# Kernel tuning notes

Measured on AMD Instinct MI355X. Metric: run time of the kernel, lower is better.

## Reference

```python
import jax, jax.numpy as jnp
import numpy as np

B, T, D, H, DH, FF = 512, 64, 512, 8, 64, 2048
SCALE = DH ** -0.5  # head_dim ** -0.5


def _ln(x, g, b):
    m = x.mean(-1, keepdims=True)
    v = x.var(-1, keepdims=True)
    return (x - m) / jnp.sqrt(v + 1e-5) * g + b


def _l2n(x):
    return x / jnp.maximum(jnp.linalg.norm(x, axis=-1, keepdims=True), 1e-12)


def setup_inputs() -> dict:
    key = jax.random.key(0)
    ks = jax.random.split(key, 16)

    def w(k, shape):
        fan_in = shape[0]
        return jax.random.normal(k, shape, jnp.float32) / np.sqrt(fan_in).astype(np.float32)

    return {
        'item_seq': jax.random.normal(ks[0], (B, T, D), jnp.float32),
        'user_static_emb': jax.random.normal(ks[1], (B, D), jnp.float32),
        'last_item_emb': jax.random.normal(ks[2], (B, D), jnp.float32),
        'init_state': jnp.zeros((B, H, DH, DH), jnp.float32),
        'Wq': w(ks[3], (D, D)), 'Wk': w(ks[4], (D, D)), 'Wv': w(ks[5], (D, D)),
        'Wa': w(ks[6], (D, H)), 'ba': jnp.zeros((H,), jnp.float32),
        'We': w(ks[7], (D, H)), 'be': jnp.zeros((H,), jnp.float32),
        'mcW1': w(ks[8], (2 * D, D)), 'mcb1': jnp.zeros((D,), jnp.float32),
        'mcg': jnp.ones((D,), jnp.float32), 'mcbt': jnp.zeros((D,), jnp.float32),
        'mcW2': w(ks[9], (D, 2 * D + 2 * H)), 'mcb2': jnp.zeros((2 * D + 2 * H,), jnp.float32),
        'Wo': w(ks[10], (D, D)), 'bo': jnp.zeros((D,), jnp.float32),
        'W1': w(ks[11], (D, FF)), 'b1': jnp.zeros((FF,), jnp.float32),
        'W2': w(ks[12], (FF, D)), 'b2': jnp.zeros((D,), jnp.float32),
        'n1g': jnp.ones((D,), jnp.float32), 'n1b': jnp.zeros((D,), jnp.float32),
        'n2g': jnp.ones((D,), jnp.float32), 'n2b': jnp.zeros((D,), jnp.float32),
    }


def reference(item_seq, user_static_emb, last_item_emb, init_state,
              Wq, Wk, Wv, Wa, ba, We, be,
              mcW1, mcb1, mcg, mcbt, mcW2, mcb2,
              Wo, bo, W1, b1, W2, b2, n1g, n1b, n2g, n2b):
    def read(q_emb, state):
        # q: (B,H,Dh) L2-normalized; read = S @ q per head
        q = _l2n((q_emb @ Wq).reshape(-1, H, DH))
        return jnp.einsum('bhij,bhj->bhi', state, q).reshape(-1, D)

    us_norm = _ln(user_static_emb, n1g, n1b)  # constant across steps

    def step(state, item):
        i_norm = _ln(item, n1g, n1b)
        mem_ctx = read(i_norm, state)
        meta_in = jnp.concatenate([us_norm, mem_ctx], axis=-1)
        h = jax.nn.relu(_ln(meta_in @ mcW1 + mcb1, mcg, mcbt))
        mo = h @ mcW2 + mcb2
        gamma, beta = mo[:, :D], mo[:, D:2 * D]
        alpha_bias, eta_bias = mo[:, 2 * D:2 * D + H], mo[:, 2 * D + H:]
        mod = i_norm * (1.0 + jnp.tanh(gamma)) + beta
        k = _l2n((mod @ Wk).reshape(-1, H, DH))
        v = (mod @ Wv).reshape(-1, H, DH)
        alpha = jax.nn.sigmoid(mod @ Wa + ba + alpha_bias)[:, :, None, None]
        eta = (jax.nn.sigmoid(mod @ We + be + eta_bias) * SCALE)[:, :, None, None]
        pred = jnp.einsum('bhij,bhj->bhi', state, k)
        upd = jnp.einsum('bhi,bhj->bhij', v - pred, k)  # rank-1 outer-product write
        return (1.0 - alpha) * state + eta * upd, None

    state, _ = jax.lax.scan(step, init_state, jnp.swapaxes(item_seq, 0, 1))

    # predict (read) path
    q_norm = _ln(last_item_emb, n1g, n1b)
    attn = read(q_norm, state) @ Wo + bo
    x = user_static_emb + attn
    x2 = _ln(x, n2g, n2b)
    ffn = jax.nn.relu(x2 @ W1 + b1) @ W2 + b2
    return x + ffn
```

## Files before the change

kernel.cpp:

```cpp
#include <hip/hip_runtime.h>
#include <cmath>

constexpr int cB = 512, cT = 64, cD = 512, cH = 8, cDH = 64, cFF = 2048;
constexpr float cSCALE = 0.125f;

typedef short bfrag __attribute__((ext_vector_type(8)));
typedef float f32x4 __attribute__((ext_vector_type(4)));

__device__ __forceinline__ short f2bf(float x) {
  union { float f; unsigned u; } v{x};
  unsigned r = v.u + 0x7fff + ((v.u >> 16) & 1);
  return (short)(r >> 16);
}
__device__ __forceinline__ float bf2f(short s) {
  union { unsigned u; float f; } v;
  v.u = ((unsigned)(unsigned short)s) << 16;
  return v.f;
}
__device__ __forceinline__ float sigm(float z) { return 1.f / (1.f + __expf(-z)); }

enum GemmMode { MQ = 0, MWO, MFF1, MFF2 };

struct GemmArgs {
  const float *A, *A2, *sm, *sr, *g, *b;
  const short *WT, *WT2;
  const float *bias, *extra;
  float *O;
  short *Os;
};

template<int MODE>
__device__ __forceinline__ float loadA(const GemmArgs& p, int r, int k) {
  if constexpr (MODE == MQ) {
    int t = r >> 9, bb = r & 511;
    float v = (t < cT) ? p.A[((size_t)bb * cT + t) * cD + k]
                       : p.A2[(size_t)bb * cD + k];
    return (v - p.sm[r]) * p.sr[r] * p.g[k] + p.b[k];
  } else if constexpr (MODE == MFF1) {
    return (p.A[(size_t)r * cD + k] - p.sm[r]) * p.sr[r] * p.g[k] + p.b[k];
  } else if constexpr (MODE == MFF2) {
    return p.A[(size_t)r * cFF + k];
  } else {
    return p.A[(size_t)r * cD + k];
  }
}

template<int MODE>
__device__ __forceinline__ void epi(const GemmArgs& p, int r, int cn, float acc) {
  if constexpr (MODE == MQ) {
    p.Os[(size_t)r * cD + cn] = f2bf(acc);
  } else if constexpr (MODE == MWO) {
    p.O[(size_t)r * cD + cn] = p.extra[(size_t)r * cD + cn] + acc + p.bias[cn];
  } else if constexpr (MODE == MFF1) {
    p.O[(size_t)r * cFF + cn] = fmaxf(acc + p.bias[cn], 0.f);
  } else {
    p.O[(size_t)r * cD + cn] = p.extra[(size_t)r * cD + cn] + acc + p.bias[cn];
  }
}

template<int MODE, int LDW>
__global__ __launch_bounds__(256) void mgemm(GemmArgs p, int K) {
  __shared__ short As[64][32];
  __shared__ short Bs[64][32];
  const int tid = threadIdx.x;
  const int lane = tid & 63, wid = tid >> 6;
  const int wm = wid & 1, wn = wid >> 1;
  const int l15 = lane & 15, qd = lane >> 4;
  const int row0 = blockIdx.x * 64;
  const int n0 = blockIdx.y * 64;

  f32x4 acc[2][2] = {};
  const int sm = tid >> 2;
  const int sk = (tid & 3) * 8;

  for (int k0 = 0; k0 < K; k0 += 32) {
    {
      short tmp[8];
#pragma unroll
      for (int j = 0; j < 8; ++j)
        tmp[j] = f2bf(loadA<MODE>(p, row0 + sm, k0 + sk + j));
      *((bfrag*)&As[sm][0] + (sk >> 3)) = *(bfrag*)tmp;
    }
    *((bfrag*)&Bs[sm][0] + (sk >> 3)) =
        *(const bfrag*)(p.WT + (size_t)(n0 + sm) * LDW + k0 + sk);
    __syncthreads();
    bfrag a0 = *((bfrag*)&As[wm * 32 + l15][0] + qd);
    bfrag a1 = *((bfrag*)&As[wm * 32 + 16 + l15][0] + qd);
    bfrag b0 = *((bfrag*)&Bs[wn * 32 + l15][0] + qd);
    bfrag b1 = *((bfrag*)&Bs[wn * 32 + 16 + l15][0] + qd);
    acc[0][0] = __builtin_amdgcn_mfma_f32_16x16x32_bf16(a0, b0, acc[0][0], 0, 0, 0);
    acc[0][1] = __builtin_amdgcn_mfma_f32_16x16x32_bf16(a0, b1, acc[0][1], 0, 0, 0);
    acc[1][0] = __builtin_amdgcn_mfma_f32_16x16x32_bf16(a1, b0, acc[1][0], 0, 0, 0);
    acc[1][1] = __builtin_amdgcn_mfma_f32_16x16x32_bf16(a1, b1, acc[1][1], 0, 0, 0);
    __syncthreads();
  }

#pragma unroll
  for (int fm = 0; fm < 2; ++fm)
#pragma unroll
    for (int fn = 0; fn < 2; ++fn)
#pragma unroll
      for (int rg = 0; rg < 4; ++rg)
        epi<MODE>(p, row0 + wm * 32 + fm * 16 + qd * 4 + rg,
                  n0 + wn * 32 + fn * 16 + l15, acc[fm][fn][rg]);
}

template<int MODE, int LDW>
__global__ __launch_bounds__(256) void pgemm(GemmArgs p, int K) {
  __shared__ short Ah[64][32], Al[64][32];
  __shared__ short Bh[64][32], Bl[64][32];
  const int tid = threadIdx.x;
  const int lane = tid & 63, wid = tid >> 6;
  const int wm = wid & 1, wn = wid >> 1;
  const int l15 = lane & 15, qd = lane >> 4;
  const int row0 = blockIdx.x * 64;
  const int n0 = blockIdx.y * 64;

  f32x4 acc[2][2] = {};
  const int sm = tid >> 2;
  const int sk = (tid & 3) * 8;

  for (int k0 = 0; k0 < K; k0 += 32) {
    {
      short th[8], tl[8];
#pragma unroll
      for (int j = 0; j < 8; ++j) {
        float a = loadA<MODE>(p, row0 + sm, k0 + sk + j);
        short h = f2bf(a);
        th[j] = h;
        tl[j] = f2bf(a - bf2f(h));
      }
      *((bfrag*)&Ah[sm][0] + (sk >> 3)) = *(bfrag*)th;
      *((bfrag*)&Al[sm][0] + (sk >> 3)) = *(bfrag*)tl;
    }
    *((bfrag*)&Bh[sm][0] + (sk >> 3)) =
        *(const bfrag*)(p.WT + (size_t)(n0 + sm) * LDW + k0 + sk);
    *((bfrag*)&Bl[sm][0] + (sk >> 3)) =
        *(const bfrag*)(p.WT2 + (size_t)(n0 + sm) * LDW + k0 + sk);
    __syncthreads();
#pragma unroll
    for (int fm = 0; fm < 2; ++fm) {
      bfrag ah = *((bfrag*)&Ah[wm * 32 + fm * 16 + l15][0] + qd);
      bfrag al = *((bfrag*)&Al[wm * 32 + fm * 16 + l15][0] + qd);
#pragma unroll
      for (int fn = 0; fn < 2; ++fn) {
        bfrag bh = *((bfrag*)&Bh[wn * 32 + fn * 16 + l15][0] + qd);
        bfrag bl = *((bfrag*)&Bl[wn * 32 + fn * 16 + l15][0] + qd);
        acc[fm][fn] = __builtin_amdgcn_mfma_f32_16x16x32_bf16(al, bh, acc[fm][fn], 0, 0, 0);
        acc[fm][fn] = __builtin_amdgcn_mfma_f32_16x16x32_bf16(ah, bl, acc[fm][fn], 0, 0, 0);
        acc[fm][fn] = __builtin_amdgcn_mfma_f32_16x16x32_bf16(ah, bh, acc[fm][fn], 0, 0, 0);
      }
    }
    __syncthreads();
  }

#pragma unroll
  for (int fm = 0; fm < 2; ++fm)
#pragma unroll
    for (int fn = 0; fn < 2; ++fn)
#pragma unroll
      for (int rg = 0; rg < 4; ++rg)
        epi<MODE>(p, row0 + wm * 32 + fm * 16 + qd * 4 + rg,
                  n0 + wn * 32 + fn * 16 + l15, acc[fm][fn][rg]);
}

__global__ __launch_bounds__(256) void tconv(const float* __restrict__ W,
                                             short* __restrict__ WT, int K, int N) {
  __shared__ float tile[32][33];
  int k0 = blockIdx.x * 32, n0 = blockIdx.y * 32;
  int tx = threadIdx.x & 31, ty = threadIdx.x >> 5;
#pragma unroll
  for (int j = 0; j < 32; j += 8) {
    int k = k0 + ty + j, n = n0 + tx;
    tile[ty + j][tx] = (k < K && n < N) ? W[(size_t)k * N + n] : 0.f;
  }
  __syncthreads();
#pragma unroll
  for (int j = 0; j < 32; j += 8) {
    int n = n0 + ty + j, k = k0 + tx;
    if (n < N && k < K) WT[(size_t)n * K + k] = f2bf(tile[tx][ty + j]);
  }
}

__global__ __launch_bounds__(256) void tconv2(const float* __restrict__ W,
                                              short* __restrict__ WTh,
                                              short* __restrict__ WTl, int K, int N) {
  __shared__ float tile[32][33];
  int k0 = blockIdx.x * 32, n0 = blockIdx.y * 32;
  int tx = threadIdx.x & 31, ty = threadIdx.x >> 5;
#pragma unroll
  for (int j = 0; j < 32; j += 8) {
    int k = k0 + ty + j, n = n0 + tx;
    tile[ty + j][tx] = (k < K && n < N) ? W[(size_t)k * N + n] : 0.f;
  }
  __syncthreads();
#pragma unroll
  for (int j = 0; j < 32; j += 8) {
    int n = n0 + ty + j, k = k0 + tx;
    if (n < N && k < K) {
      float v = tile[tx][ty + j];
      short h = f2bf(v);
      WTh[(size_t)n * K + k] = h;
      WTl[(size_t)n * K + k] = f2bf(v - bf2f(h));
    }
  }
}

__global__ __launch_bounds__(256) void ln_stats_k(
    const float* __restrict__ item_seq, const float* __restrict__ last_item,
    const float* __restrict__ user, const float* __restrict__ n1g,
    const float* __restrict__ n1b, float* __restrict__ lnm,
    float* __restrict__ lnr, float* __restrict__ us_norm) {
  const int lane = threadIdx.x & 63;
  const int w = blockIdx.x * 4 + (threadIdx.x >> 6);
  const float* src;
  int cls, bi = 0;
  if (w < cT * cB) {
    int t = w >> 9, bb = w & 511;
    src = item_seq + ((size_t)bb * cT + t) * cD;
    cls = 0;
  } else if (w < cT * cB + cB) {
    bi = w - cT * cB;
    src = last_item + (size_t)bi * cD;
    cls = 1;
  } else {
    bi = w - cT * cB - cB;
    src = user + (size_t)bi * cD;
    cls = 2;
  }
  float x[8], s = 0.f, ss = 0.f;
#pragma unroll
  for (int i = 0; i < 8; ++i) {
    float v = src[lane + i * 64];
    x[i] = v; s += v; ss += v * v;
  }
#pragma unroll
  for (int o = 32; o >= 1; o >>= 1) { s += __shfl_xor(s, o); ss += __shfl_xor(ss, o); }
  float m = s * (1.f / cD);
  float rstd = rsqrtf(ss * (1.f / cD) - m * m + 1e-5f);
  if (cls == 0) {
    if (lane == 0) { lnm[w] = m; lnr[w] = rstd; }
  } else if (cls == 1) {
    if (lane == 0) { lnm[cT * cB + bi] = m; lnr[cT * cB + bi] = rstd; }
  } else {
#pragma unroll
    for (int i = 0; i < 8; ++i) {
      int d = lane + i * 64;
      us_norm[(size_t)bi * cD + d] = (x[i] - m) * rstd * n1g[d] + n1b[d];
    }
  }
}

__global__ __launch_bounds__(256) void row_stats_k(const float* __restrict__ X,
                                                   float* __restrict__ M,
                                                   float* __restrict__ R) {
  const int lane = threadIdx.x & 63;
  const int w = blockIdx.x * 4 + (threadIdx.x >> 6);
  float s = 0.f, ss = 0.f;
#pragma unroll
  for (int i = 0; i < 8; ++i) {
    float v = X[(size_t)w * cD + lane + i * 64];
    s += v; ss += v * v;
  }
#pragma unroll
  for (int o = 32; o >= 1; o >>= 1) { s += __shfl_xor(s, o); ss += __shfl_xor(ss, o); }
  if (lane == 0) {
    float m = s * (1.f / cD);
    M[w] = m;
    R[w] = rsqrtf(ss * (1.f / cD) - m * m + 1e-5f);
  }
}

struct Scan2Params {
  const float *item_seq, *init_state, *us_norm, *lnm, *lnr, *n1g, *n1b;
  const float *mcb1, *mcg, *mcbt, *mcb2, *ba, *be;
  const short *wt_m1, *wt_m2, *wt_k, *wt_v, *wt_ae, *q_all;
  float *mem_ctx;
};

__device__ __forceinline__ bfrag mk_afrag(const float* xr, int kc, int qd) {
  const float* s = xr + kc * 32 + qd * 8;
  float4 a = *(const float4*)s;
  float4 b = *(const float4*)(s + 4);
  short t[8] = {f2bf(a.x), f2bf(a.y), f2bf(a.z), f2bf(a.w),
                f2bf(b.x), f2bf(b.y), f2bf(b.z), f2bf(b.w)};
  return *(bfrag*)t;
}

__global__ __launch_bounds__(1024, 4) void scan2_k(Scan2Params p) {
  const int tid = threadIdx.x;
  const int lane = tid & 63, w = tid >> 6;
  const int bb = w >> 3, h = w & 7;
  const int l15 = lane & 15, qd = lane >> 4;
  const int b0 = blockIdx.x * 2;

  __shared__ float xcat[2][1024];
  __shared__ float rbuf[2][512];
  __shared__ float x2b[2][512];
  __shared__ float mo[2][1040];
  __shared__ float modv[2][512];
  __shared__ float kvb[2][1024];
  __shared__ float khat[16][64];
  __shared__ float qh[16][64];
  __shared__ float aeta[2][8][2];
  __shared__ float st[2][2], st2[2][2];
  __shared__ float cb1[512], cg[512], cbt[512], cb2[1040];
  __shared__ float cn1g[512], cn1b[512], cba[8], cbe[8];

  if (tid < 512) {
    cb1[tid] = p.mcb1[tid]; cg[tid] = p.mcg[tid]; cbt[tid] = p.mcbt[tid];
    cn1g[tid] = p.n1g[tid]; cn1b[tid] = p.n1b[tid];
  }
  cb2[tid] = p.mcb2[tid];
  if (tid < 16) cb2[1024 + tid] = p.mcb2[1024 + tid];
  if (tid < 8) { cba[tid] = p.ba[tid]; cbe[tid] = p.be[tid]; }
  {
    int row = tid >> 9, c = tid & 511;
    xcat[row][c] = p.us_norm[(size_t)(b0 + row) * cD + c];
  }

  float S[64];
  {
    const float* sp = p.init_state + ((((size_t)(b0 + bb)) * cH + h) * cDH + lane) * cDH;
#pragma unroll
    for (int j = 0; j < 64; j += 4) {
      float4 t4 = *(const float4*)(sp + j);
      S[j] = t4.x; S[j + 1] = t4.y; S[j + 2] = t4.z; S[j + 3] = t4.w;
    }
  }
  float memv;
  {
    float qv = bf2f(p.q_all[(size_t)(b0 + bb) * cD + h * cDH + lane]);
    float qs = qv * qv;
#pragma unroll
    for (int o = 32; o >= 1; o >>= 1) qs += __shfl_xor(qs, o);
    qh[w][lane] = qv / fmaxf(sqrtf(qs), 1e-12f);
    memv = 0.f;
#pragma unroll
    for (int j = 0; j < 64; j += 4) {
      float4 q4 = *(const float4*)&qh[w][j];
      memv += S[j] * q4.x + S[j + 1] * q4.y + S[j + 2] * q4.z + S[j + 3] * q4.w;
    }
    xcat[bb][512 + h * cDH + lane] = memv;
  }
  __syncthreads();

  for (int t = 0; t < cT; ++t) {
    {
      f32x4 a0 = {}, a1 = {};
      const int n0 = w * 16, n1 = (w + 16) * 16;
#pragma unroll 4
      for (int kc = 0; kc < 32; ++kc) {
        bfrag A = {};
        if (l15 < 2) A = mk_afrag(&xcat[l15][0], kc, qd);
        bfrag B0 = *(const bfrag*)(p.wt_m1 + (size_t)(n0 + l15) * 1024 + kc * 32 + qd * 8);
        bfrag B1 = *(const bfrag*)(p.wt_m1 + (size_t)(n1 + l15) * 1024 + kc * 32 + qd * 8);
        a0 = __builtin_amdgcn_mfma_f32_16x16x32_bf16(A, B0, a0, 0, 0, 0);
        a1 = __builtin_amdgcn_mfma_f32_16x16x32_bf16(A, B1, a1, 0, 0, 0);
      }
      if (lane < 16) {
        rbuf[0][n0 + lane] = a0[0] + cb1[n0 + lane];
        rbuf[1][n0 + lane] = a0[1] + cb1[n0 + lane];
        rbuf[0][n1 + lane] = a1[0] + cb1[n1 + lane];
        rbuf[1][n1 + lane] = a1[1] + cb1[n1 + lane];
      }
    }
    __syncthreads();
    if (w < 2) {
      float s = 0.f, ss = 0.f;
#pragma unroll
      for (int i = 0; i < 8; ++i) { float v = rbuf[w][lane + i * 64]; s += v; ss += v * v; }
#pragma unroll
      for (int o = 32; o >= 1; o >>= 1) { s += __shfl_xor(s, o); ss += __shfl_xor(ss, o); }
      if (lane == 0) {
        float m = s * (1.f / cD);
        st[w][0] = m;
        st[w][1] = rsqrtf(ss * (1.f / cD) - m * m + 1e-5f);
      }
    } else if (w == 2 && lane < 2) {
      st2[lane][0] = p.lnm[t * cB + b0 + lane];
      st2[lane][1] = p.lnr[t * cB + b0 + lane];
    }
    __syncthreads();
    {
      int row = tid >> 9, c = tid & 511;
      x2b[row][c] = fmaxf((rbuf[row][c] - st[row][0]) * st[row][1] * cg[c] + cbt[c], 0.f);
    }
    __syncthreads();
    {
      f32x4 acc[4] = {};
#pragma unroll 2
      for (int kc = 0; kc < 16; ++kc) {
        bfrag A = {};
        if (l15 < 2) A = mk_afrag(&x2b[l15][0], kc, qd);
#pragma unroll
        for (int tI = 0; tI < 4; ++tI) {
          int n0 = (tI * 16 + w) * 16;
          bfrag B = *(const bfrag*)(p.wt_m2 + (size_t)(n0 + l15) * 512 + kc * 32 + qd * 8);
          acc[tI] = __builtin_amdgcn_mfma_f32_16x16x32_bf16(A, B, acc[tI], 0, 0, 0);
        }
      }
      if (lane < 16)
#pragma unroll
        for (int tI = 0; tI < 4; ++tI) {
          int n0 = (tI * 16 + w) * 16;
          mo[0][n0 + lane] = acc[tI][0] + cb2[n0 + lane];
          mo[1][n0 + lane] = acc[tI][1] + cb2[n0 + lane];
        }
      if (w == 0) {
        f32x4 e = {};
        for (int kc = 0; kc < 16; ++kc) {
          bfrag A = {};
          if (l15 < 2) A = mk_afrag(&x2b[l15][0], kc, qd);
          bfrag B = *(const bfrag*)(p.wt_m2 + (size_t)(1024 + l15) * 512 + kc * 32 + qd * 8);
          e = __builtin_amdgcn_mfma_f32_16x16x32_bf16(A, B, e, 0, 0, 0);
        }
        if (lane < 16) {
          mo[0][1024 + lane] = e[0] + cb2[1024 + lane];
          mo[1][1024 + lane] = e[1] + cb2[1024 + lane];
        }
      }
    }
    __syncthreads();
    {
      int row = tid >> 9, c = tid & 511;
      float inm = (p.item_seq[(((size_t)(b0 + row)) * cT + t) * cD + c] - st2[row][0]) *
                      st2[row][1] * cn1g[c] + cn1b[c];
      modv[row][c] = inm * (1.f + tanhf(mo[row][c])) + mo[row][512 + c];
    }
    __syncthreads();
    {
      f32x4 acc[4] = {};
#pragma unroll 2
      for (int kc = 0; kc < 16; ++kc) {
        bfrag A = {};
        if (l15 < 2) A = mk_afrag(&modv[l15][0], kc, qd);
#pragma unroll
        for (int tI = 0; tI < 4; ++tI) {
          int tile = tI * 16 + w;
          const short* wt = (tile < 32) ? p.wt_k : p.wt_v;
          int n0 = ((tile < 32) ? tile : tile - 32) * 16;
          bfrag B = *(const bfrag*)(wt + (size_t)(n0 + l15) * 512 + kc * 32 + qd * 8);
          acc[tI] = __builtin_amdgcn_mfma_f32_16x16x32_bf16(A, B, acc[tI], 0, 0, 0);
        }
      }
      if (lane < 16)
#pragma unroll
        for (int tI = 0; tI < 4; ++tI) {
          int tile = tI * 16 + w;
          int dst = (tile < 32) ? tile * 16 + lane : 512 + (tile - 32) * 16 + lane;
          kvb[0][dst] = acc[tI][0];
          kvb[1][dst] = acc[tI][1];
        }
      if (w == 0) {
        f32x4 e = {};
        for (int kc = 0; kc < 16; ++kc) {
          bfrag A = {};
          if (l15 < 2) A = mk_afrag(&modv[l15][0], kc, qd);
          bfrag B = *(const bfrag*)(p.wt_ae + (size_t)l15 * 512 + kc * 32 + qd * 8);
          e = __builtin_amdgcn_mfma_f32_16x16x32_bf16(A, B, e, 0, 0, 0);
        }
        if (lane < 16) {
          if (lane < 8) {
            int hh = lane;
            aeta[0][hh][0] = sigm(e[0] + cba[hh] + mo[0][1024 + hh]);
            aeta[1][hh][0] = sigm(e[1] + cba[hh] + mo[1][1024 + hh]);
          } else {
            int hh = lane - 8;
            aeta[0][hh][1] = cSCALE * sigm(e[0] + cbe[hh] + mo[0][1032 + hh]);
            aeta[1][hh][1] = cSCALE * sigm(e[1] + cbe[hh] + mo[1][1032 + hh]);
          }
        }
      }
    }
    __syncthreads();
    {
      float kvv = kvb[bb][h * cDH + lane];
      float ks = kvv * kvv;
#pragma unroll
      for (int o = 32; o >= 1; o >>= 1) ks += __shfl_xor(ks, o);
      khat[w][lane] = kvv / fmaxf(sqrtf(ks), 1e-12f);
      float qv = bf2f(p.q_all[((size_t)(t + 1) * cB + (b0 + bb)) * cD + h * cDH + lane]);
      float qs = qv * qv;
#pragma unroll
      for (int o = 32; o >= 1; o >>= 1) qs += __shfl_xor(qs, o);
      qh[w][lane] = qv / fmaxf(sqrtf(qs), 1e-12f);

      float vv = kvb[bb][512 + h * cDH + lane];
      float al = aeta[bb][h][0], et = aeta[bb][h][1];
      float pred = 0.f;
#pragma unroll
      for (int j = 0; j < 64; j += 4) {
        float4 k4 = *(const float4*)&khat[w][j];
        pred += S[j] * k4.x + S[j + 1] * k4.y + S[j + 2] * k4.z + S[j + 3] * k4.w;
      }
      float f = et * (vv - pred), oma = 1.f - al;
      memv = 0.f;
#pragma unroll
      for (int j = 0; j < 64; j += 4) {
        float4 k4 = *(const float4*)&khat[w][j];
        float4 q4 = *(const float4*)&qh[w][j];
        S[j]     = oma * S[j]     + f * k4.x; memv += S[j]     * q4.x;
        S[j + 1] = oma * S[j + 1] + f * k4.y; memv += S[j + 1] * q4.y;
        S[j + 2] = oma * S[j + 2] + f * k4.z; memv += S[j + 2] * q4.z;
        S[j + 3] = oma * S[j + 3] + f * k4.w; memv += S[j + 3] * q4.w;
      }
      xcat[bb][512 + h * cDH + lane] = memv;
    }
    __syncthreads();
  }

  p.mem_ctx[(size_t)(b0 + bb) * cD + h * cDH + lane] = memv;
}

extern "C" void kernel_launch(void* const* d_in, const int* in_sizes, int n_in,
                              void* d_out, int out_size, void* d_ws, size_t ws_size,
                              hipStream_t stream) {
  (void)in_sizes; (void)n_in; (void)out_size;
  const float* item_seq   = (const float*)d_in[0];
  const float* user_stat  = (const float*)d_in[1];
  const float* last_item  = (const float*)d_in[2];
  const float* init_state = (const float*)d_in[3];
  const float* Wq  = (const float*)d_in[4];
  const float* Wk  = (const float*)d_in[5];
  const float* Wv  = (const float*)d_in[6];
  const float* Wa  = (const float*)d_in[7];
  const float* ba  = (const float*)d_in[8];
  const float* We  = (const float*)d_in[9];
  const float* be  = (const float*)d_in[10];
  const float* mcW1 = (const float*)d_in[11];
  const float* mcb1 = (const float*)d_in[12];
  const float* mcg  = (const float*)d_in[13];
  const float* mcbt = (const float*)d_in[14];
  const float* mcW2 = (const float*)d_in[15];
  const float* mcb2 = (const float*)d_in[16];
  const float* Wo  = (const float*)d_in[17];
  const float* bo  = (const float*)d_in[18];
  const float* W1  = (const float*)d_in[19];
  const float* b1  = (const float*)d_in[20];
  const float* W2  = (const float*)d_in[21];
  const float* b2  = (const float*)d_in[22];
  const float* n1g = (const float*)d_in[23];
  const float* n1b = (const float*)d_in[24];
  const float* n2g = (const float*)d_in[25];
  const float* n2b = (const float*)d_in[26];

  float* ws = (float*)d_ws;
  size_t off = 0;
  auto alloc = [&](size_t n) { float* p = ws + off; off += n; return p; };
  auto salloc = [&](size_t n) { return (short*)alloc((n + 1) / 2); };

  short* q_all   = salloc((size_t)(cT + 1) * cB * cD);
  float* lnm     = alloc((size_t)(cT + 1) * cB);
  float* lnr     = alloc((size_t)(cT + 1) * cB);
  float* us_norm = alloc((size_t)cB * cD);
  float* mem_ctx = alloc((size_t)cB * cD);
  float* x_buf   = alloc((size_t)cB * cD);
  float* xm      = alloc(cB);
  float* xr      = alloc(cB);
  float* u_buf   = alloc((size_t)cB * cFF);
  short* wt_q    = salloc((size_t)512 * 512);
  short* wt_m1   = salloc((size_t)512 * 1024);
  short* wt_m2   = salloc((size_t)1040 * 512);
  short* wt_k    = salloc((size_t)512 * 512);
  short* wt_v    = salloc((size_t)512 * 512);
  short* wt_ae   = salloc((size_t)16 * 512);
  short* wt_o    = salloc((size_t)512 * 512);
  short* wt_o_l  = salloc((size_t)512 * 512);
  short* wt_1    = salloc((size_t)2048 * 512);
  short* wt_1_l  = salloc((size_t)2048 * 512);
  short* wt_2    = salloc((size_t)512 * 2048);
  short* wt_2_l  = salloc((size_t)512 * 2048);
  if (ws_size < off * sizeof(float)) return;

  tconv<<<dim3(16, 16), 256, 0, stream>>>(Wq, wt_q, 512, 512);
  tconv<<<dim3(32, 16), 256, 0, stream>>>(mcW1, wt_m1, 1024, 512);
  tconv<<<dim3(16, 33), 256, 0, stream>>>(mcW2, wt_m2, 512, 1040);
  tconv<<<dim3(16, 16), 256, 0, stream>>>(Wk, wt_k, 512, 512);
  tconv<<<dim3(16, 16), 256, 0, stream>>>(Wv, wt_v, 512, 512);
  tconv<<<dim3(16, 1), 256, 0, stream>>>(Wa, wt_ae, 512, 8);
  tconv<<<dim3(16, 1), 256, 0, stream>>>(We, wt_ae + (size_t)8 * 512, 512, 8);
  tconv2<<<dim3(16, 16), 256, 0, stream>>>(Wo, wt_o, wt_o_l, 512, 512);
  tconv2<<<dim3(16, 64), 256, 0, stream>>>(W1, wt_1, wt_1_l, 512, 2048);
  tconv2<<<dim3(64, 16), 256, 0, stream>>>(W2, wt_2, wt_2_l, 2048, 512);

  ln_stats_k<<<(cT * cB + 2 * cB) / 4, 256, 0, stream>>>(
      item_seq, last_item, user_stat, n1g, n1b, lnm, lnr, us_norm);

  {
    GemmArgs p{}; p.A = item_seq; p.A2 = last_item; p.sm = lnm; p.sr = lnr;
    p.g = n1g; p.b = n1b; p.WT = wt_q; p.Os = q_all;
    mgemm<MQ, 512><<<dim3(520, 8), 256, 0, stream>>>(p, 512);
  }

  {
    Scan2Params sp{};
    sp.item_seq = item_seq; sp.init_state = init_state; sp.us_norm = us_norm;
    sp.lnm = lnm; sp.lnr = lnr; sp.n1g = n1g; sp.n1b = n1b;
    sp.mcb1 = mcb1; sp.mcg = mcg; sp.mcbt = mcbt; sp.mcb2 = mcb2;
    sp.ba = ba; sp.be = be;
    sp.wt_m1 = wt_m1; sp.wt_m2 = wt_m2; sp.wt_k = wt_k; sp.wt_v = wt_v;
    sp.wt_ae = wt_ae; sp.q_all = q_all;
    sp.mem_ctx = mem_ctx;
    scan2_k<<<dim3(cB / 2), dim3(1024), 0, stream>>>(sp);
  }

  {
    GemmArgs p{}; p.A = mem_ctx; p.WT = wt_o; p.WT2 = wt_o_l;
    p.bias = bo; p.extra = user_stat; p.O = x_buf;
    pgemm<MWO, 512><<<dim3(8, 8), 256, 0, stream>>>(p, 512);
  }
  row_stats_k<<<cB / 4, 256, 0, stream>>>(x_buf, xm, xr);
  {
    GemmArgs p{}; p.A = x_buf; p.sm = xm; p.sr = xr; p.g = n2g; p.b = n2b;
    p.WT = wt_1; p.WT2 = wt_1_l; p.bias = b1; p.O = u_buf;
    pgemm<MFF1, 512><<<dim3(8, 32), 256, 0, stream>>>(p, 512);
  }
  {
    GemmArgs p{}; p.A = u_buf; p.WT = wt_2; p.WT2 = wt_2_l;
    p.bias = b2; p.extra = x_buf; p.O = (float*)d_out;
    pgemm<MFF2, 2048><<<dim3(8, 8), 256, 0, stream>>>(p, 2048);
  }
}
```

Before: 7.095 ms.

## Process one batch row per 512-thread block in the recurrent scan kernel

Restructures the scan kernel so each block handles a single batch row with 8 waves (one per head) instead of two rows with 16 waves, launching twice as many smaller blocks. Each wave now computes four output tiles per GEMM stage instead of two. Nontemporal loads are used for the initial state and item sequence. This aims to improve block scheduling and reduce per-step barrier cost, but it halves useful rows per MFMA and doubles total weight streaming from cache across the batch.

```diff
diff --git a/kernel.cpp b/kernel.cpp
--- a/kernel.cpp
+++ b/kernel.cpp
@@ -287,50 +287,45 @@
   return *(bfrag*)t;
 }
 
-__global__ __launch_bounds__(1024, 4) void scan2_k(Scan2Params p) {
+__global__ __launch_bounds__(512, 4) void scan1_k(Scan2Params p) {
   const int tid = threadIdx.x;
   const int lane = tid & 63, w = tid >> 6;
-  const int bb = w >> 3, h = w & 7;
   const int l15 = lane & 15, qd = lane >> 4;
-  const int b0 = blockIdx.x * 2;
-
-  __shared__ float xcat[2][1024];
-  __shared__ float rbuf[2][512];
-  __shared__ float x2b[2][512];
-  __shared__ float mo[2][1040];
-  __shared__ float modv[2][512];
-  __shared__ float kvb[2][1024];
-  __shared__ float khat[16][64];
-  __shared__ float qh[16][64];
-  __shared__ float aeta[2][8][2];
-  __shared__ float st[2][2], st2[2][2];
+  const int b = blockIdx.x;
+
+  __shared__ float xcat[1024];
+  __shared__ float rbuf[512];
+  __shared__ float x2b[512];
+  __shared__ float mo[1040];
+  __shared__ float modv[512];
+  __shared__ float kvb[1024];
+  __shared__ float khat[8][64];
+  __shared__ float qh[8][64];
+  __shared__ float aeta[8][2];
+  __shared__ float st[2];
   __shared__ float cb1[512], cg[512], cbt[512], cb2[1040];
   __shared__ float cn1g[512], cn1b[512], cba[8], cbe[8];
 
-  if (tid < 512) {
-    cb1[tid] = p.mcb1[tid]; cg[tid] = p.mcg[tid]; cbt[tid] = p.mcbt[tid];
-    cn1g[tid] = p.n1g[tid]; cn1b[tid] = p.n1b[tid];
-  }
+  cb1[tid] = p.mcb1[tid]; cg[tid] = p.mcg[tid]; cbt[tid] = p.mcbt[tid];
+  cn1g[tid] = p.n1g[tid]; cn1b[tid] = p.n1b[tid];
   cb2[tid] = p.mcb2[tid];
+  cb2[512 + tid] = p.mcb2[512 + tid];
   if (tid < 16) cb2[1024 + tid] = p.mcb2[1024 + tid];
   if (tid < 8) { cba[tid] = p.ba[tid]; cbe[tid] = p.be[tid]; }
-  {
-    int row = tid >> 9, c = tid & 511;
-    xcat[row][c] = p.us_norm[(size_t)(b0 + row) * cD + c];
-  }
+  xcat[tid] = p.us_norm[(size_t)b * cD + tid];
 
   float S[64];
   {
-    const float* sp = p.init_state + ((((size_t)(b0 + bb)) * cH + h) * cDH + lane) * cDH;
+    const float* sp = p.init_state + ((((size_t)b) * cH + w) * cDH + lane) * cDH;
 #pragma unroll
     for (int j = 0; j < 64; j += 4) {
-      float4 t4 = *(const float4*)(sp + j);
-      S[j] = t4.x; S[j + 1] = t4.y; S[j + 2] = t4.z; S[j + 3] = t4.w;
+      f32x4 t4 = __builtin_nontemporal_load((const f32x4*)(sp + j));
+      S[j] = t4[0]; S[j + 1] = t4[1]; S[j + 2] = t4[2]; S[j + 3] = t4[3];
     }
   }
   float memv;
   {
-    float qv = bf2f(p.q_all[(size_t)(b0 + bb) * cD + h * cDH + lane]);
+    float qv = bf2f(p.q_all[(size_t)b * cD + w * cDH + lane]);
     float qs = qv * qv;
 #pragma unroll
     for (int o = 32; o >= 1; o >>= 1) qs += __shfl_xor(qs, o);
@@ -341,153 +336,147 @@
       float4 q4 = *(const float4*)&qh[w][j];
       memv += S[j] * q4.x + S[j + 1] * q4.y + S[j + 2] * q4.z + S[j + 3] * q4.w;
     }
-    xcat[bb][512 + h * cDH + lane] = memv;
+    xcat[512 + w * cDH + lane] = memv;
   }
   __syncthreads();
 
   for (int t = 0; t < cT; ++t) {
     {
-      f32x4 a0 = {}, a1 = {};
-      const int n0 = w * 16, n1 = (w + 16) * 16;
+      f32x4 acc[4] = {};
 #pragma unroll 4
       for (int kc = 0; kc < 32; ++kc) {
         bfrag A = {};
-        if (l15 < 2) A = mk_afrag(&xcat[l15][0], kc, qd);
-        bfrag B0 = *(const bfrag*)(p.wt_m1 + (size_t)(n0 + l15) * 1024 + kc * 32 + qd * 8);
-        bfrag B1 = *(const bfrag*)(p.wt_m1 + (size_t)(n1 + l15) * 1024 + kc * 32 + qd * 8);
-        a0 = __builtin_amdgcn_mfma_f32_16x16x32_bf16(A, B0, a0, 0, 0, 0);
-        a1 = __builtin_amdgcn_mfma_f32_16x16x32_bf16(A, B1, a1, 0, 0, 0);
-      }
-      if (lane < 16) {
-        rbuf[0][n0 + lane] = a0[0] + cb1[n0 + lane];
-        rbuf[1][n0 + lane] = a0[1] + cb1[n0 + lane];
-        rbuf[0][n1 + lane] = a1[0] + cb1[n1 + lane];
-        rbuf[1][n1 + lane] = a1[1] + cb1[n1 + lane];
-      }
-    }
-    __syncthreads();
-    if (w < 2) {
+        if (l15 == 0) A = mk_afrag(xcat, kc, qd);
+#pragma unroll
+        for (int i = 0; i < 4; ++i) {
+          int n0 = (w * 4 + i) * 16;
+          bfrag B = *(const bfrag*)(p.wt_m1 + (size_t)(n0 + l15) * 1024 + kc * 32 + qd * 8);
+          acc[i] = __builtin_amdgcn_mfma_f32_16x16x32_bf16(A, B, acc[i], 0, 0, 0);
+        }
+      }
+      if (lane < 16)
+#pragma unroll
+        for (int i = 0; i < 4; ++i) {
+          int n0 = (w * 4 + i) * 16;
+          rbuf[n0 + lane] = acc[i][0] + cb1[n0 + lane];
+        }
+    }
+    __syncthreads();
+    if (w == 0) {
       float s = 0.f, ss = 0.f;
 #pragma unroll
-      for (int i = 0; i < 8; ++i) { float v = rbuf[w][lane + i * 64]; s += v; ss += v * v; }
+      for (int i = 0; i < 8; ++i) { float v = rbuf[lane + i * 64]; s += v; ss += v * v; }
 #pragma unroll
       for (int o = 32; o >= 1; o >>= 1) { s += __shfl_xor(s, o); ss += __shfl_xor(ss, o); }
       if (lane == 0) {
         float m = s * (1.f / cD);
-        st[w][0] = m;
-        st[w][1] = rsqrtf(ss * (1.f / cD) - m * m + 1e-5f);
-      }
-    } else if (w == 2 && lane < 2) {
-      st2[lane][0] = p.lnm[t * cB + b0 + lane];
-      st2[lane][1] = p.lnr[t * cB + b0 + lane];
-    }
+        st[0] = m;
+        st[1] = rsqrtf(ss * (1.f / cD) - m * m + 1e-5f);
+      }
+    }
+    __syncthreads();
+    x2b[tid] = fmaxf((rbuf[tid] - st[0]) * st[1] * cg[tid] + cbt[tid], 0.f);
     __syncthreads();
     {
-      int row = tid >> 9, c = tid & 511;
-      x2b[row][c] = fmaxf((rbuf[row][c] - st[row][0]) * st[row][1] * cg[c] + cbt[c], 0.f);
-    }
-    __syncthreads();
-    {
-      f32x4 acc[4] = {};
+#pragma unroll
+      for (int hb = 0; hb < 2; ++hb) {
+        f32x4 acc[4] = {};
 #pragma unroll 2
-      for (int kc = 0; kc < 16; ++kc) {
-        bfrag A = {};
-        if (l15 < 2) A = mk_afrag(&x2b[l15][0], kc, qd);
-#pragma unroll
-        for (int tI = 0; tI < 4; ++tI) {
-          int n0 = (tI * 16 + w) * 16;
-          bfrag B = *(const bfrag*)(p.wt_m2 + (size_t)(n0 + l15) * 512 + kc * 32 + qd * 8);
-          acc[tI] = __builtin_amdgcn_mfma_f32_16x16x32_bf16(A, B, acc[tI], 0, 0, 0);
+        for (int kc = 0; kc < 16; ++kc) {
+          bfrag A = {};
+          if (l15 == 0) A = mk_afrag(x2b, kc, qd);
+#pragma unroll
+          for (int i = 0; i < 4; ++i) {
+            int n0 = (hb * 32 + w * 4 + i) * 16;
+            bfrag B = *(const bfrag*)(p.wt_m2 + (size_t)(n0 + l15) * 512 + kc * 32 + qd * 8);
+            acc[i] = __builtin_amdgcn_mfma_f32_16x16x32_bf16(A, B, acc[i], 0, 0, 0);
+          }
         }
-      }
-      if (lane < 16)
-#pragma unroll
-        for (int tI = 0; tI < 4; ++tI) {
-          int n0 = (tI * 16 + w) * 16;
-          mo[0][n0 + lane] = acc[tI][0] + cb2[n0 + lane];
-          mo[1][n0 + lane] = acc[tI][1] + cb2[n0 + lane];
-        }
-      if (w == 0) {
+        if (lane < 16)
+#pragma unroll
+          for (int i = 0; i < 4; ++i) {
+            int n0 = (hb * 32 + w * 4 + i) * 16;
+            mo[n0 + lane] = acc[i][0] + cb2[n0 + lane];
+          }
+      }
+      if (w == 7) {
         f32x4 e = {};
         for (int kc = 0; kc < 16; ++kc) {
           bfrag A = {};
-          if (l15 < 2) A = mk_afrag(&x2b[l15][0], kc, qd);
+          if (l15 == 0) A = mk_afrag(x2b, kc, qd);
           bfrag B = *(const bfrag*)(p.wt_m2 + (size_t)(1024 + l15) * 512 + kc * 32 + qd * 8);
           e = __builtin_amdgcn_mfma_f32_16x16x32_bf16(A, B, e, 0, 0, 0);
         }
-        if (lane < 16) {
-          mo[0][1024 + lane] = e[0] + cb2[1024 + lane];
-          mo[1][1024 + lane] = e[1] + cb2[1024 + lane];
+        if (lane < 16) mo[1024 + lane] = e[0] + cb2[1024 + lane];
+      }
+    }
+    __syncthreads();
+    {
+      float m2 = p.lnm[(size_t)t * cB + b];
+      float r2 = p.lnr[(size_t)t * cB + b];
+      float iv = __builtin_nontemporal_load(
+          p.item_seq + (((size_t)b) * cT + t) * cD + tid);
+      float inm = (iv - m2) * r2 * cn1g[tid] + cn1b[tid];
+      modv[tid] = inm * (1.f + tanhf(mo[tid])) + mo[512 + tid];
+    }
+    __syncthreads();
+    {
+#pragma unroll
+      for (int hb = 0; hb < 2; ++hb) {
+        const short* wt = hb ? p.wt_v : p.wt_k;
+        const int base = hb ? 512 : 0;
+        f32x4 acc[4] = {};
+#pragma unroll 2
+        for (int kc = 0; kc < 16; ++kc) {
+          bfrag A = {};
+          if (l15 == 0) A = mk_afrag(modv, kc, qd);
+#pragma unroll
+          for (int i = 0; i < 4; ++i) {
+            int n0 = (w * 4 + i) * 16;
+            bfrag B = *(const bfrag*)(wt + (size_t)(n0 + l15) * 512 + kc * 32 + qd * 8);
+            acc[i] = __builtin_amdgcn_mfma_f32_16x16x32_bf16(A, B, acc[i], 0, 0, 0);
+          }
         }
-      }
-    }
-    __syncthreads();
-    {
-      int row = tid >> 9, c = tid & 511;
-      float inm = (p.item_seq[(((size_t)(b0 + row)) * cT + t) * cD + c] - st2[row][0]) *
-                      st2[row][1] * cn1g[c] + cn1b[c];
-      modv[row][c] = inm * (1.f + tanhf(mo[row][c])) + mo[row][512 + c];
-    }
-    __syncthreads();
-    {
-      f32x4 acc[4] = {};
-#pragma unroll 2
-      for (int kc = 0; kc < 16; ++kc) {
-        bfrag A = {};
-        if (l15 < 2) A = mk_afrag(&modv[l15][0], kc, qd);
-#pragma unroll
-        for (int tI = 0; tI < 4; ++tI) {
-          int tile = tI * 16 + w;
-          const short* wt = (tile < 32) ? p.wt_k : p.wt_v;
-          int n0 = ((tile < 32) ? tile : tile - 32) * 16;
-          bfrag B = *(const bfrag*)(wt + (size_t)(n0 + l15) * 512 + kc * 32 + qd * 8);
-          acc[tI] = __builtin_amdgcn_mfma_f32_16x16x32_bf16(A, B, acc[tI], 0, 0, 0);
-        }
-      }
-      if (lane < 16)
-#pragma unroll
-        for (int tI = 0; tI < 4; ++tI) {
-          int tile = tI * 16 + w;
-          int dst = (tile < 32) ? tile * 16 + lane : 512 + (tile - 32) * 16 + lane;
-          kvb[0][dst] = acc[tI][0];
-          kvb[1][dst] = acc[tI][1];
-        }
-      if (w == 0) {
+        if (lane < 16)
+#pragma unroll
+          for (int i = 0; i < 4; ++i) {
+            int n0 = (w * 4 + i) * 16;
+            kvb[base + n0 + lane] = acc[i][0];
+          }
+      }
+      if (w == 7) {
         f32x4 e = {};
         for (int kc = 0; kc < 16; ++kc) {
           bfrag A = {};
-          if (l15 < 2) A = mk_afrag(&modv[l15][0], kc, qd);
+          if (l15 == 0) A = mk_afrag(modv, kc, qd);
           bfrag B = *(const bfrag*)(p.wt_ae + (size_t)l15 * 512 + kc * 32 + qd * 8);
           e = __builtin_amdgcn_mfma_f32_16x16x32_bf16(A, B, e, 0, 0, 0);
         }
         if (lane < 16) {
           if (lane < 8) {
-            int hh = lane;
-            aeta[0][hh][0] = sigm(e[0] + cba[hh] + mo[0][1024 + hh]);
-            aeta[1][hh][0] = sigm(e[1] + cba[hh] + mo[1][1024 + hh]);
+            aeta[lane][0] = sigm(e[0] + cba[lane] + mo[1024 + lane]);
           } else {
             int hh = lane - 8;
-            aeta[0][hh][1] = cSCALE * sigm(e[0] + cbe[hh] + mo[0][1032 + hh]);
-            aeta[1][hh][1] = cSCALE * sigm(e[1] + cbe[hh] + mo[1][1032 + hh]);
+            aeta[hh][1] = cSCALE * sigm(e[0] + cbe[hh] + mo[1032 + hh]);
           }
         }
       }
     }
     __syncthreads();
     {
-      float kvv = kvb[bb][h * cDH + lane];
+      float kvv = kvb[w * cDH + lane];
       float ks = kvv * kvv;
 #pragma unroll
       for (int o = 32; o >= 1; o >>= 1) ks += __shfl_xor(ks, o);
       khat[w][lane] = kvv / fmaxf(sqrtf(ks), 1e-12f);
-      float qv = bf2f(p.q_all[((size_t)(t + 1) * cB + (b0 + bb)) * cD + h * cDH + lane]);
+      float qv = bf2f(p.q_all[((size_t)(t + 1) * cB + b) * cD + w * cDH + lane]);
       float qs = qv * qv;
 #pragma unroll
       for (int o = 32; o >= 1; o >>= 1) qs += __shfl_xor(qs, o);
       qh[w][lane] = qv / fmaxf(sqrtf(qs), 1e-12f);
 
-      float vv = kvb[bb][512 + h * cDH + lane];
-      float al = aeta[bb][h][0], et = aeta[bb][h][1];
+      float vv = kvb[512 + w * cDH + lane];
+      float al = aeta[w][0], et = aeta[w][1];
       float pred = 0.f;
 #pragma unroll
       for (int j = 0; j < 64; j += 4) {
@@ -505,12 +494,12 @@
         S[j + 2] = oma * S[j + 2] + f * k4.z; memv += S[j + 2] * q4.z;
         S[j + 3] = oma * S[j + 3] + f * k4.w; memv += S[j + 3] * q4.w;
       }
-      xcat[bb][512 + h * cDH + lane] = memv;
-    }
-    __syncthreads();
-  }
-
-  p.mem_ctx[(size_t)(b0 + bb) * cD + h * cDH + lane] = memv;
+      xcat[512 + w * cDH + lane] = memv;
+    }
+    __syncthreads();
+  }
+
+  p.mem_ctx[(size_t)b * cD + w * cDH + lane] = memv;
 }
 
 extern "C" void kernel_launch(void* const* d_in, const int* in_sizes, int n_in,
@@ -602,7 +591,7 @@
     sp.wt_m1 = wt_m1; sp.wt_m2 = wt_m2; sp.wt_k = wt_k; sp.wt_v = wt_v;
     sp.wt_ae = wt_ae; sp.q_all = q_all;
     sp.mem_ctx = mem_ctx;
-    scan2_k<<<dim3(cB / 2), dim3(1024), 0, stream>>>(sp);
+    scan1_k<<<dim3(cB), dim3(512), 0, stream>>>(sp);
   }
 
   {
```

After: 12.36 ms. 74.1% more time.
